# Performance work log

Hardware: AMD Instinct MI355X
Metric: run time of the kernel (lower is better)

## Reference

```python
import jax, jax.numpy as jnp
import numpy as np

N = 8192
F_IN = 690
F_OUT = 690
H = 3
ALPHA = 0.2  # LeakyReLU negative slope
NEG_INF = -9e15


def setup_inputs() -> dict:
    key = jax.random.key(0)
    k1, k2, k3, k4 = jax.random.split(key, 4)
    x = jax.random.normal(k1, (N, F_IN), dtype=jnp.float32)
    adj = jax.random.randint(k2, (N, N), 0, 2, dtype=jnp.int32)
    adj = adj.at[jnp.arange(N), jnp.arange(N)].set(1)  # self-loops, as in eye() init
    # Xavier-ish scaled params, stacked over heads
    W = jax.random.normal(k3, (H, F_IN, F_OUT), dtype=jnp.float32) * 0.05
    a = jax.random.normal(k4, (H, 2 * F_OUT, 1), dtype=jnp.float32) * 0.05
    return {"x": x, "adj": adj, "W": W, "a": a}


def reference(x, adj, W, a):
    # Wh per head: [H, N, F_OUT]
    Wh = jnp.einsum('nf,hfo->hno', x, W)
    # Additive decomposition of concat-based score: e_ij = leakyrelu(a1_i + a2_j)
    a1 = jnp.einsum('hno,ho->hn', Wh, a[:, :F_OUT, 0])  # [H, N]
    a2 = jnp.einsum('hno,ho->hn', Wh, a[:, F_OUT:, 0])  # [H, N]
    e = jax.nn.leaky_relu(a1[:, :, None] + a2[:, None, :], negative_slope=ALPHA)  # [H, N, N]
    e = jnp.where(adj[None, :, :] > 0, e, NEG_INF)
    attn = jax.nn.softmax(e, axis=-1)
    h_prime = jnp.einsum('hnm,hmo->hno', attn, Wh)  # [H, N, F_OUT]
    # GAT(concat=False): mean over heads, then ELU (dropout is identity in eval)
    y = jax.nn.elu(jnp.mean(h_prime, axis=0))  # [N, F_OUT]
    return y
```

## Files before the change

kernel.cpp:

```cpp
#include <hip/hip_runtime.h>
#include <hip/hip_bf16.h>
#include <stdint.h>

#define NN 8192
#define FD 690
#define NH 3
#define KPAD 704
#define OPAD 768
#define USTRIDE 704
#define KS 2
#define LOG2E 1.4426950408889634f

typedef __attribute__((ext_vector_type(8))) short bf16x8;
typedef __attribute__((ext_vector_type(4))) float f32x4;

typedef __attribute__((address_space(1))) const void gas_t;
typedef __attribute__((address_space(3))) void las_t;

__device__ __forceinline__ void async_ld16(const void* g, void* l) {
  __builtin_amdgcn_global_load_lds((gas_t*)g, (las_t*)l, 16, 0, 0);
}

__device__ __forceinline__ float bf2f(unsigned short u) {
  return __uint_as_float(((unsigned int)u) << 16);
}
__device__ __forceinline__ unsigned short f2bf(float f) {
  __hip_bfloat16 h = __float2bfloat16(f);
  return *reinterpret_cast<unsigned short*>(&h);
}
__device__ __forceinline__ float selbit(float e, uint32_t lo, uint32_t hi) {
  uint64_t m = ((uint64_t)hi << 32) | lo;
  float r;
  asm("v_cndmask_b32 %0, 0, %1, %2" : "=v"(r) : "v"(e), "s"(m));
  return r;
}

__global__ __launch_bounds__(256) void k_cast_x(const float* __restrict__ x,
                                                unsigned short* __restrict__ xb) {
  int idx = blockIdx.x * 256 + threadIdx.x;
  if (idx >= NN * KPAD) return;
  int n = idx / KPAD, f = idx - n * KPAD;
  float v = (f < FD) ? x[(size_t)n * FD + f] : 0.f;
  xb[idx] = f2bf(v);
}

__global__ __launch_bounds__(256) void k_cast_wt(const float* __restrict__ W,
                                                 unsigned short* __restrict__ wt) {
  int idx = blockIdx.x * 256 + threadIdx.x;
  if (idx >= NH * OPAD * KPAD) return;
  int h = idx / (OPAD * KPAD);
  int rem = idx - h * OPAD * KPAD;
  int o = rem / KPAD, f = rem - o * KPAD;
  float v = (o < FD && f < FD) ? W[((size_t)h * FD + f) * FD + o] : 0.f;
  wt[idx] = f2bf(v);
}

__global__ __launch_bounds__(256) void k_pack(const int* __restrict__ adj,
                                              uint64_t* __restrict__ bm) {
  int wid = (blockIdx.x * 256 + threadIdx.x) >> 6;
  int lane = threadIdx.x & 63;
  int i = wid >> 7, wj = wid & 127;
  int v = adj[(int64_t)i * NN + wj * 64 + lane];
  uint64_t m = __ballot(v > 0);
  if (lane == 0) bm[i * 128 + wj] = m;
}

__global__ __launch_bounds__(512) void k_gemm_wht(const unsigned short* __restrict__ wt,
                                                  const unsigned short* __restrict__ xb,
                                                  const float* __restrict__ a,
                                                  unsigned short* __restrict__ wht,
                                                  float* __restrict__ a1acc,
                                                  float* __restrict__ a2acc) {
  const int m0 = blockIdx.x * 128;
  const int n0 = blockIdx.y * 256;
  const int h  = blockIdx.z;
  const int tid = threadIdx.x;
  const int w = tid >> 6, l = tid & 63;
  const int wm = w >> 2, wn = w & 3;
  __shared__ unsigned short As[128 * 64];
  __shared__ unsigned short Bs[256 * 64];
  const unsigned short* Ag = wt + (size_t)h * OPAD * KPAD;
  f32x4 acc[4][4] = {};
  for (int kt = 0; kt < KPAD / 64; ++kt) {
    const int k0 = kt * 64;
#pragma unroll
    for (int r = 0; r < 2; ++r) {
      const unsigned short* g = Ag + (size_t)(m0 + r * 64 + w * 8 + (l >> 3)) * KPAD + k0 + (l & 7) * 8;
      async_ld16(g, &As[(r * 64 + w * 8) * 64]);
    }
#pragma unroll
    for (int r = 0; r < 4; ++r) {
      const unsigned short* g = xb + (size_t)(n0 + r * 64 + w * 8 + (l >> 3)) * KPAD + k0 + (l & 7) * 8;
      async_ld16(g, &Bs[(r * 64 + w * 8) * 64]);
    }
    __syncthreads();
#pragma unroll
    for (int ks = 0; ks < 2; ++ks) {
      bf16x8 af[4], bfr[4];
#pragma unroll
      for (int mi = 0; mi < 4; ++mi)
        af[mi] = *reinterpret_cast<const bf16x8*>(
            &As[(wm * 64 + mi * 16 + (l & 15)) * 64 + ks * 32 + (l >> 4) * 8]);
#pragma unroll
      for (int ni = 0; ni < 4; ++ni)
        bfr[ni] = *reinterpret_cast<const bf16x8*>(
            &Bs[(wn * 64 + ni * 16 + (l & 15)) * 64 + ks * 32 + (l >> 4) * 8]);
#pragma unroll
      for (int mi = 0; mi < 4; ++mi)
#pragma unroll
        for (int ni = 0; ni < 4; ++ni)
          acc[mi][ni] = __builtin_amdgcn_mfma_f32_16x16x32_bf16(af[mi], bfr[ni], acc[mi][ni], 0, 0, 0);
    }
    __syncthreads();
  }
  unsigned short* Wh = wht + (size_t)h * OPAD * NN;
#pragma unroll
  for (int mi = 0; mi < 4; ++mi)
#pragma unroll
    for (int j = 0; j < 4; ++j) {
      int o = m0 + wm * 64 + mi * 16 + (l >> 4) * 4 + j;
#pragma unroll
      for (int ni = 0; ni < 4; ++ni) {
        int n = n0 + wn * 64 + ni * 16 + (l & 15);
        float val = (o == FD) ? 1.0f : acc[mi][ni][j];
        Wh[(size_t)o * NN + n] = f2bf(val);
      }
    }
  const float* ap1 = a + h * 2 * FD;
  const float* ap2 = ap1 + FD;
  float av1[4][4], av2[4][4];
#pragma unroll
  for (int mi = 0; mi < 4; ++mi)
#pragma unroll
    for (int j = 0; j < 4; ++j) {
      int o = m0 + wm * 64 + mi * 16 + (l >> 4) * 4 + j;
      bool ok = (o < FD);
      av1[mi][j] = ok ? ap1[o] : 0.f;
      av2[mi][j] = ok ? ap2[o] : 0.f;
    }
#pragma unroll
  for (int ni = 0; ni < 4; ++ni) {
    float p1 = 0.f, p2 = 0.f;
#pragma unroll
    for (int mi = 0; mi < 4; ++mi)
#pragma unroll
      for (int j = 0; j < 4; ++j) {
        p1 += acc[mi][ni][j] * av1[mi][j];
        p2 += acc[mi][ni][j] * av2[mi][j];
      }
    int n = n0 + wn * 64 + ni * 16 + (l & 15);
    unsafeAtomicAdd(&a1acc[h * NN + n], p1);
    unsafeAtomicAdd(&a2acc[h * NN + n], p2);
  }
}

__global__ __launch_bounds__(256) void k_exp(const float* __restrict__ a1acc,
                                             const float* __restrict__ a2acc,
                                             float* __restrict__ e1s, float* __restrict__ f1s,
                                             float* __restrict__ e2s, float* __restrict__ f2s) {
  int i = blockIdx.x * 256 + threadIdx.x;
  if (i >= NH * NN) return;
  float s1 = a1acc[i] * LOG2E, s2 = a2acc[i] * LOG2E;
  e1s[i] = exp2f(s1);
  f1s[i] = exp2f(0.2f * s1);
  e2s[i] = exp2f(s2);
  f2s[i] = exp2f(0.2f * s2);
}

__global__ __launch_bounds__(512, 4) void k_pv(const unsigned short* __restrict__ wht,
                                               const float* __restrict__ e1s,
                                               const float* __restrict__ f1s,
                                               const float* __restrict__ e2s,
                                               const float* __restrict__ f2s,
                                               const uint64_t* __restrict__ bm,
                                               float* __restrict__ U) {
  const int m0 = blockIdx.x * 64;
  const int n0 = blockIdx.y * 384;
  const int h    = blockIdx.z / KS;
  const int kseg = blockIdx.z % KS;
  const int tid = threadIdx.x;
  const int w = tid >> 6, l = tid & 63;
  const int wu = __builtin_amdgcn_readfirstlane(w);
  __shared__ unsigned short As[64 * 64];
  __shared__ unsigned short Bs[384 * 64];
  const unsigned short* Bg = wht + (size_t)h * OPAD * NN;
  const uint64_t* bmw = bm + (size_t)(m0 + wu * 8) * 128;
  float E1v[8], F1v[8];
#pragma unroll
  for (int r = 0; r < 8; ++r) {
    E1v[r] = e1s[h * NN + m0 + wu * 8 + r];
    F1v[r] = f1s[h * NN + m0 + wu * 8 + r];
  }

  const int kt0 = kseg * (NN / 64 / KS);
  const int ktend = kt0 + NN / 64 / KS;

  f32x4 acc[4][3] = {};

  for (int kt = kt0; kt < ktend; ++kt) {
    const int k0 = kt * 64;
    const float e2v = e2s[h * NN + k0 + l];
    const float f2v = f2s[h * NN + k0 + l];
#pragma unroll
    for (int call = 0; call < 6; ++call) {
      int c = call * 512 + tid;
      int row = c >> 3;
      int kb  = c & 7;
      int kbs = kb ^ (row & 7);
      const unsigned short* g = Bg + (size_t)(n0 + row) * NN + k0 + kbs * 8;
      async_ld16(g, &Bs[(size_t)c * 8]);
    }
#pragma unroll
    for (int r = 0; r < 8; ++r) {
      uint64_t mrow = bmw[(size_t)r * 128 + kt];
      uint32_t mlo = __builtin_amdgcn_readfirstlane((uint32_t)mrow);
      uint32_t mhi = __builtin_amdgcn_readfirstlane((uint32_t)(mrow >> 32));
      float e = fmaxf(E1v[r] * e2v, F1v[r] * f2v);
      e = selbit(e, mlo, mhi);
      As[(wu * 8 + r) * 64 + (l ^ (r << 3))] = f2bf(e);
    }
    __syncthreads();

#pragma unroll
    for (int ks = 0; ks < 2; ++ks) {
      bf16x8 af[4], bfr[3];
#pragma unroll
      for (int mi = 0; mi < 4; ++mi) {
        int row = mi * 16 + (l & 15);
        af[mi] = *reinterpret_cast<const bf16x8*>(
            &As[row * 64 + (((ks * 4 + (l >> 4)) ^ (row & 7)) * 8)]);
      }
#pragma unroll
      for (int ni = 0; ni < 3; ++ni) {
        int row = w * 48 + ni * 16 + (l & 15);
        bfr[ni] = *reinterpret_cast<const bf16x8*>(
            &Bs[row * 64 + (((ks * 4 + (l >> 4)) ^ (row & 7)) * 8)]);
      }
#pragma unroll
      for (int mi = 0; mi < 4; ++mi)
#pragma unroll
        for (int ni = 0; ni < 3; ++ni)
          acc[mi][ni] = __builtin_amdgcn_mfma_f32_16x16x32_bf16(af[mi], bfr[ni], acc[mi][ni], 0, 0, 0);
    }
    __syncthreads();
  }

#pragma unroll
  for (int mi = 0; mi < 4; ++mi)
#pragma unroll
    for (int j = 0; j < 4; ++j) {
      int i = m0 + mi * 16 + (l >> 4) * 4 + j;
#pragma unroll
      for (int ni = 0; ni < 3; ++ni) {
        int n = n0 + w * 48 + ni * 16 + (l & 15);
        if (n <= FD) unsafeAtomicAdd(&U[((size_t)h * NN + i) * USTRIDE + n], acc[mi][ni][j]);
      }
    }
}

__global__ __launch_bounds__(256) void k_final(const float* __restrict__ U,
                                               float* __restrict__ y) {
  int idx = blockIdx.x * 256 + threadIdx.x;
  if (idx >= NN * FD) return;
  int i = idx / FD, o = idx - i * FD;
  const size_t HS = (size_t)NN * USTRIDE;
  float s = 0.f;
#pragma unroll
  for (int h = 0; h < NH; ++h) {
    size_t b = h * HS + (size_t)i * USTRIDE;
    s += U[b + o] / U[b + FD];
  }
  s *= (1.f / 3.f);
  y[idx] = s > 0.f ? s : (expf(s) - 1.f);
}

extern "C" void kernel_launch(void* const* d_in, const int* in_sizes, int n_in,
                              void* d_out, int out_size, void* d_ws, size_t ws_size,
                              hipStream_t stream) {
  const float* x   = (const float*)d_in[0];
  const int*   adj = (const int*)d_in[1];
  const float* W   = (const float*)d_in[2];
  const float* a   = (const float*)d_in[3];
  float* y = (float*)d_out;

  char* ws = (char*)d_ws;
  size_t off = 0;
  auto alloc = [&](size_t bytes) {
    void* p = ws + off;
    off = (off + bytes + 255) & ~(size_t)255;
    return p;
  };
  unsigned short* xb  = (unsigned short*)alloc((size_t)NN * KPAD * 2);
  unsigned short* wt  = (unsigned short*)alloc((size_t)NH * OPAD * KPAD * 2);
  unsigned short* wht = (unsigned short*)alloc((size_t)NH * OPAD * NN * 2);
  float* e1s = (float*)alloc((size_t)NH * NN * 4);
  float* f1s = (float*)alloc((size_t)NH * NN * 4);
  float* e2s = (float*)alloc((size_t)NH * NN * 4);
  float* f2s = (float*)alloc((size_t)NH * NN * 4);
  uint64_t* bm = (uint64_t*)alloc((size_t)NN * 128 * 8);
  float* U = (float*)alloc((size_t)NH * NN * USTRIDE * 4);
  float* a1acc = (float*)alloc((size_t)NH * NN * 4);
  float* a2acc = (float*)alloc((size_t)NH * NN * 4);
  (void)ws_size; (void)in_sizes; (void)n_in; (void)out_size;

  hipMemsetAsync(U, 0, (size_t)NH * NN * USTRIDE * 4, stream);
  hipMemsetAsync(a1acc, 0, (size_t)NH * NN * 4 * 2, stream);

  k_cast_x<<<(NN * KPAD + 255) / 256, 256, 0, stream>>>(x, xb);
  k_cast_wt<<<(NH * OPAD * KPAD + 255) / 256, 256, 0, stream>>>(W, wt);
  k_pack<<<NN * 128 / 4, 256, 0, stream>>>(adj, bm);
  k_gemm_wht<<<dim3(OPAD / 128, NN / 256, NH), 512, 0, stream>>>(wt, xb, a, wht, a1acc, a2acc);
  k_exp<<<(NH * NN + 255) / 256, 256, 0, stream>>>(a1acc, a2acc, e1s, f1s, e2s, f2s);
  k_pv<<<dim3(NN / 64, 2, NH * KS), 512, 0, stream>>>(wht, e1s, f1s, e2s, f2s, bm, U);
  k_final<<<(NN * FD + 255) / 256, 256, 0, stream>>>(U, y);
}
```

Measured before the change: 643.0 us.

## Drop split-K, double-buffer A tile, and load B fragments directly from global

Removes the K split in the attention-times-Wh kernel so each block owns a full row range and writes results with plain stores, eliminating atomics and the zero-fill memset of U. The softmax-weight tile is generated into a double-buffered LDS array one step ahead, halving barriers per iteration. B fragments are now read straight from global memory into registers rather than staged through LDS. This trades LDS traffic and atomics for exposed global load latency and half as many blocks.

```diff
diff --git a/kernel.cpp b/kernel.cpp
--- a/kernel.cpp
+++ b/kernel.cpp
@@ -8,7 +8,6 @@
 #define KPAD 704
 #define OPAD 768
 #define USTRIDE 704
-#define KS 2
 #define LOG2E 1.4426950408889634f
 
 typedef __attribute__((ext_vector_type(8))) short bf16x8;
@@ -176,13 +175,11 @@
                                                float* __restrict__ U) {
   const int m0 = blockIdx.x * 64;
   const int n0 = blockIdx.y * 384;
-  const int h    = blockIdx.z / KS;
-  const int kseg = blockIdx.z % KS;
+  const int h  = blockIdx.z;
   const int tid = threadIdx.x;
   const int w = tid >> 6, l = tid & 63;
   const int wu = __builtin_amdgcn_readfirstlane(w);
-  __shared__ unsigned short As[64 * 64];
-  __shared__ unsigned short Bs[384 * 64];
+  __shared__ unsigned short As[2][64 * 64];
   const unsigned short* Bg = wht + (size_t)h * OPAD * NN;
   const uint64_t* bmw = bm + (size_t)(m0 + wu * 8) * 128;
   float E1v[8], F1v[8];
@@ -191,25 +188,12 @@
     E1v[r] = e1s[h * NN + m0 + wu * 8 + r];
     F1v[r] = f1s[h * NN + m0 + wu * 8 + r];
   }
-
-  const int kt0 = kseg * (NN / 64 / KS);
-  const int ktend = kt0 + NN / 64 / KS;
-
-  f32x4 acc[4][3] = {};
-
-  for (int kt = kt0; kt < ktend; ++kt) {
-    const int k0 = kt * 64;
-    const float e2v = e2s[h * NN + k0 + l];
-    const float f2v = f2s[h * NN + k0 + l];
-#pragma unroll
-    for (int call = 0; call < 6; ++call) {
-      int c = call * 512 + tid;
-      int row = c >> 3;
-      int kb  = c & 7;
-      int kbs = kb ^ (row & 7);
-      const unsigned short* g = Bg + (size_t)(n0 + row) * NN + k0 + kbs * 8;
-      async_ld16(g, &Bs[(size_t)c * 8]);
-    }
+  const unsigned short* bptr[3];
+#pragma unroll
+  for (int ni = 0; ni < 3; ++ni)
+    bptr[ni] = Bg + (size_t)(n0 + w * 48 + ni * 16 + (l & 15)) * NN + (l >> 4) * 8;
+
+  auto genA = [&](int buf, int kt, float e2v, float f2v) {
 #pragma unroll
     for (int r = 0; r < 8; ++r) {
       uint64_t mrow = bmw[(size_t)r * 128 + kt];
@@ -217,24 +201,40 @@
       uint32_t mhi = __builtin_amdgcn_readfirstlane((uint32_t)(mrow >> 32));
       float e = fmaxf(E1v[r] * e2v, F1v[r] * f2v);
       e = selbit(e, mlo, mhi);
-      As[(wu * 8 + r) * 64 + (l ^ (r << 3))] = f2bf(e);
-    }
+      As[buf][(wu * 8 + r) * 64 + (l ^ (r << 3))] = f2bf(e);
+    }
+  };
+
+  f32x4 acc[4][3] = {};
+
+  float e2c = e2s[h * NN + l];
+  float f2c = f2s[h * NN + l];
+  genA(0, 0, e2c, f2c);
+  float e2n = e2s[h * NN + 64 + l];
+  float f2n = f2s[h * NN + 64 + l];
+
+  int cur = 0;
+  for (int kt = 0; kt < 128; ++kt) {
     __syncthreads();
-
+    const int k0 = kt * 64;
+    float e2nn = 0.f, f2nn = 0.f;
+    if (kt + 2 < 128) {
+      e2nn = e2s[h * NN + (kt + 2) * 64 + l];
+      f2nn = f2s[h * NN + (kt + 2) * 64 + l];
+    }
+    if (kt + 1 < 128) genA(cur ^ 1, kt + 1, e2n, f2n);
 #pragma unroll
     for (int ks = 0; ks < 2; ++ks) {
-      bf16x8 af[4], bfr[3];
+      bf16x8 bfr[3];
+#pragma unroll
+      for (int ni = 0; ni < 3; ++ni)
+        bfr[ni] = *reinterpret_cast<const bf16x8*>(bptr[ni] + k0 + ks * 32);
+      bf16x8 af[4];
 #pragma unroll
       for (int mi = 0; mi < 4; ++mi) {
         int row = mi * 16 + (l & 15);
         af[mi] = *reinterpret_cast<const bf16x8*>(
-            &As[row * 64 + (((ks * 4 + (l >> 4)) ^ (row & 7)) * 8)]);
-      }
-#pragma unroll
-      for (int ni = 0; ni < 3; ++ni) {
-        int row = w * 48 + ni * 16 + (l & 15);
-        bfr[ni] = *reinterpret_cast<const bf16x8*>(
-            &Bs[row * 64 + (((ks * 4 + (l >> 4)) ^ (row & 7)) * 8)]);
+            &As[cur][row * 64 + (((ks * 4 + (l >> 4)) ^ (row & 7)) * 8)]);
       }
 #pragma unroll
       for (int mi = 0; mi < 4; ++mi)
@@ -242,7 +242,9 @@
         for (int ni = 0; ni < 3; ++ni)
           acc[mi][ni] = __builtin_amdgcn_mfma_f32_16x16x32_bf16(af[mi], bfr[ni], acc[mi][ni], 0, 0, 0);
     }
-    __syncthreads();
+    cur ^= 1;
+    e2n = e2nn;
+    f2n = f2nn;
   }
 
 #pragma unroll
@@ -253,7 +255,7 @@
 #pragma unroll
       for (int ni = 0; ni < 3; ++ni) {
         int n = n0 + w * 48 + ni * 16 + (l & 15);
-        if (n <= FD) unsafeAtomicAdd(&U[((size_t)h * NN + i) * USTRIDE + n], acc[mi][ni][j]);
+        if (n <= FD) U[((size_t)h * NN + i) * USTRIDE + n] = acc[mi][ni][j];
       }
     }
 }
@@ -303,7 +305,6 @@
   float* a2acc = (float*)alloc((size_t)NH * NN * 4);
   (void)ws_size; (void)in_sizes; (void)n_in; (void)out_size;
 
-  hipMemsetAsync(U, 0, (size_t)NH * NN * USTRIDE * 4, stream);
   hipMemsetAsync(a1acc, 0, (size_t)NH * NN * 4 * 2, stream);
 
   k_cast_x<<<(NN * KPAD + 255) / 256, 256, 0, stream>>>(x, xb);
@@ -311,6 +312,6 @@
   k_pack<<<NN * 128 / 4, 256, 0, stream>>>(adj, bm);
   k_gemm_wht<<<dim3(OPAD / 128, NN / 256, NH), 512, 0, stream>>>(wt, xb, a, wht, a1acc, a2acc);
   k_exp<<<(NH * NN + 255) / 256, 256, 0, stream>>>(a1acc, a2acc, e1s, f1s, e2s, f2s);
-  k_pv<<<dim3(NN / 64, 2, NH * KS), 512, 0, stream>>>(wht, e1s, f1s, e2s, f2s, bm, U);
+  k_pv<<<dim3(NN / 64, 2, NH), 512, 0, stream>>>(wht, e1s, f1s, e2s, f2s, bm, U);
   k_final<<<(NN * FD + 255) / 256, 256, 0, stream>>>(U, y);
 }
```

New measurement: 824.9 us. 28.3% more time.

## Retile attention-value GEMM to 256x128 blocks with vectorized score generation

Applied to the files above, without the earlier changes.

Reshapes the k_pv tile from 64 rows x 384 columns to 256 rows x 128 columns. Waves are arranged 4x2, the K split grows from 2 to 4 segments, and the occupancy hint drops to 2 blocks. The attention-score tile is now built with vectorized loads of e2/f2 and mask words, each lane writing four bf16 values, in place of per-row scalar writes with readfirstlane masks. The aim is more MFMA work per byte of Wh loaded. In exchange, the exp/mask scores are recomputed across 6 column blocks instead of 2, and there are twice as many atomic adds into U.

```diff
diff --git a/kernel.cpp b/kernel.cpp
--- a/kernel.cpp
+++ b/kernel.cpp
@@ -8,7 +8,7 @@
 #define KPAD 704
 #define OPAD 768
 #define USTRIDE 704
-#define KS 2
+#define KS 4
 #define LOG2E 1.4426950408889634f
 
 typedef __attribute__((ext_vector_type(8))) short bf16x8;
@@ -27,12 +27,6 @@
 __device__ __forceinline__ unsigned short f2bf(float f) {
   __hip_bfloat16 h = __float2bfloat16(f);
   return *reinterpret_cast<unsigned short*>(&h);
-}
-__device__ __forceinline__ float selbit(float e, uint32_t lo, uint32_t hi) {
-  uint64_t m = ((uint64_t)hi << 32) | lo;
-  float r;
-  asm("v_cndmask_b32 %0, 0, %1, %2" : "=v"(r) : "v"(e), "s"(m));
-  return r;
 }
 
 __global__ __launch_bounds__(256) void k_cast_x(const float* __restrict__ x,
@@ -167,42 +161,48 @@
   f2s[i] = exp2f(0.2f * s2);
 }
 
-__global__ __launch_bounds__(512, 4) void k_pv(const unsigned short* __restrict__ wht,
+__global__ __launch_bounds__(512, 2) void k_pv(const unsigned short* __restrict__ wht,
                                                const float* __restrict__ e1s,
                                                const float* __restrict__ f1s,
                                                const float* __restrict__ e2s,
                                                const float* __restrict__ f2s,
                                                const uint64_t* __restrict__ bm,
                                                float* __restrict__ U) {
-  const int m0 = blockIdx.x * 64;
-  const int n0 = blockIdx.y * 384;
+  const int m0 = blockIdx.x * 256;
+  const int n0 = blockIdx.y * 128;
   const int h    = blockIdx.z / KS;
   const int kseg = blockIdx.z % KS;
   const int tid = threadIdx.x;
   const int w = tid >> 6, l = tid & 63;
-  const int wu = __builtin_amdgcn_readfirstlane(w);
-  __shared__ unsigned short As[64 * 64];
-  __shared__ unsigned short Bs[384 * 64];
+  const int wm = w >> 1, wn = w & 1;
+  __shared__ unsigned short As[256 * 64];
+  __shared__ unsigned short Bs[128 * 64];
   const unsigned short* Bg = wht + (size_t)h * OPAD * NN;
-  const uint64_t* bmw = bm + (size_t)(m0 + wu * 8) * 128;
-  float E1v[8], F1v[8];
-#pragma unroll
-  for (int r = 0; r < 8; ++r) {
-    E1v[r] = e1s[h * NN + m0 + wu * 8 + r];
-    F1v[r] = f1s[h * NN + m0 + wu * 8 + r];
-  }
-
-  const int kt0 = kseg * (NN / 64 / KS);
-  const int ktend = kt0 + NN / 64 / KS;
-
-  f32x4 acc[4][3] = {};
+
+  float E1p[8], F1p[8];
+#pragma unroll
+  for (int s = 0; s < 8; ++s) {
+    int row = m0 + w * 32 + s * 4 + (l >> 4);
+    E1p[s] = e1s[h * NN + row];
+    F1p[s] = f1s[h * NN + row];
+  }
+
+  const int kt0 = kseg * (128 / KS);
+  const int ktend = kt0 + 128 / KS;
+
+  f32x4 acc[4][4] = {};
 
   for (int kt = kt0; kt < ktend; ++kt) {
     const int k0 = kt * 64;
-    const float e2v = e2s[h * NN + k0 + l];
-    const float f2v = f2s[h * NN + k0 + l];
-#pragma unroll
-    for (int call = 0; call < 6; ++call) {
+    const f32x4 e2v = *reinterpret_cast<const f32x4*>(&e2s[h * NN + k0 + (l & 15) * 4]);
+    const f32x4 f2v = *reinterpret_cast<const f32x4*>(&f2s[h * NN + k0 + (l & 15) * 4]);
+    uint2 mr[8];
+#pragma unroll
+    for (int s = 0; s < 8; ++s)
+      mr[s] = *reinterpret_cast<const uint2*>(
+          &bm[(size_t)(m0 + w * 32 + s * 4 + (l >> 4)) * 128 + kt]);
+#pragma unroll
+    for (int call = 0; call < 2; ++call) {
       int c = call * 512 + tid;
       int row = c >> 3;
       int kb  = c & 7;
@@ -211,36 +211,51 @@
       async_ld16(g, &Bs[(size_t)c * 8]);
     }
 #pragma unroll
-    for (int r = 0; r < 8; ++r) {
-      uint64_t mrow = bmw[(size_t)r * 128 + kt];
-      uint32_t mlo = __builtin_amdgcn_readfirstlane((uint32_t)mrow);
-      uint32_t mhi = __builtin_amdgcn_readfirstlane((uint32_t)(mrow >> 32));
-      float e = fmaxf(E1v[r] * e2v, F1v[r] * f2v);
-      e = selbit(e, mlo, mhi);
-      As[(wu * 8 + r) * 64 + (l ^ (r << 3))] = f2bf(e);
+    for (int s = 0; s < 8; ++s) {
+      int row = w * 32 + s * 4 + (l >> 4);
+      uint32_t half = ((l & 15) < 8) ? mr[s].x : mr[s].y;
+      uint32_t m4 = (half >> (((l & 15) & 7) * 4)) & 0xF;
+      uint32_t lo, hi;
+      {
+        float e0 = fmaxf(E1p[s] * e2v[0], F1p[s] * f2v[0]);
+        float e1 = fmaxf(E1p[s] * e2v[1], F1p[s] * f2v[1]);
+        e0 = (m4 & 1u) ? e0 : 0.f;
+        e1 = (m4 & 2u) ? e1 : 0.f;
+        lo = (uint32_t)f2bf(e0) | ((uint32_t)f2bf(e1) << 16);
+      }
+      {
+        float e2_ = fmaxf(E1p[s] * e2v[2], F1p[s] * f2v[2]);
+        float e3 = fmaxf(E1p[s] * e2v[3], F1p[s] * f2v[3]);
+        e2_ = (m4 & 4u) ? e2_ : 0.f;
+        e3 = (m4 & 8u) ? e3 : 0.f;
+        hi = (uint32_t)f2bf(e2_) | ((uint32_t)f2bf(e3) << 16);
+      }
+      int kb = (l & 15) >> 1;
+      int phys = kb ^ (row & 7);
+      int addr = row * 64 + phys * 8 + ((l & 15) & 1) * 4;
+      uint2 val; val.x = lo; val.y = hi;
+      *reinterpret_cast<uint2*>(&As[addr]) = val;
     }
     __syncthreads();
 
 #pragma unroll
     for (int ks = 0; ks < 2; ++ks) {
-      bf16x8 af[4], bfr[3];
+      bf16x8 bfr[4];
+#pragma unroll
+      for (int ni = 0; ni < 4; ++ni) {
+        int row = wn * 64 + ni * 16 + (l & 15);
+        int phys = (ks * 4 + (l >> 4)) ^ (row & 7);
+        bfr[ni] = *reinterpret_cast<const bf16x8*>(&Bs[row * 64 + phys * 8]);
+      }
 #pragma unroll
       for (int mi = 0; mi < 4; ++mi) {
-        int row = mi * 16 + (l & 15);
-        af[mi] = *reinterpret_cast<const bf16x8*>(
-            &As[row * 64 + (((ks * 4 + (l >> 4)) ^ (row & 7)) * 8)]);
-      }
-#pragma unroll
-      for (int ni = 0; ni < 3; ++ni) {
-        int row = w * 48 + ni * 16 + (l & 15);
-        bfr[ni] = *reinterpret_cast<const bf16x8*>(
-            &Bs[row * 64 + (((ks * 4 + (l >> 4)) ^ (row & 7)) * 8)]);
-      }
-#pragma unroll
-      for (int mi = 0; mi < 4; ++mi)
-#pragma unroll
-        for (int ni = 0; ni < 3; ++ni)
-          acc[mi][ni] = __builtin_amdgcn_mfma_f32_16x16x32_bf16(af[mi], bfr[ni], acc[mi][ni], 0, 0, 0);
+        int arow = wm * 64 + mi * 16 + (l & 15);
+        int aphys = (ks * 4 + (l >> 4)) ^ (arow & 7);
+        bf16x8 af = *reinterpret_cast<const bf16x8*>(&As[arow * 64 + aphys * 8]);
+#pragma unroll
+        for (int ni = 0; ni < 4; ++ni)
+          acc[mi][ni] = __builtin_amdgcn_mfma_f32_16x16x32_bf16(af, bfr[ni], acc[mi][ni], 0, 0, 0);
+      }
     }
     __syncthreads();
   }
@@ -249,10 +264,10 @@
   for (int mi = 0; mi < 4; ++mi)
 #pragma unroll
     for (int j = 0; j < 4; ++j) {
-      int i = m0 + mi * 16 + (l >> 4) * 4 + j;
-#pragma unroll
-      for (int ni = 0; ni < 3; ++ni) {
-        int n = n0 + w * 48 + ni * 16 + (l & 15);
+      int i = m0 + wm * 64 + mi * 16 + (l >> 4) * 4 + j;
+#pragma unroll
+      for (int ni = 0; ni < 4; ++ni) {
+        int n = n0 + wn * 64 + ni * 16 + (l & 15);
         if (n <= FD) unsafeAtomicAdd(&U[((size_t)h * NN + i) * USTRIDE + n], acc[mi][ni][j]);
       }
     }
@@ -311,6 +326,6 @@
   k_pack<<<NN * 128 / 4, 256, 0, stream>>>(adj, bm);
   k_gemm_wht<<<dim3(OPAD / 128, NN / 256, NH), 512, 0, stream>>>(wt, xb, a, wht, a1acc, a2acc);
   k_exp<<<(NH * NN + 255) / 256, 256, 0, stream>>>(a1acc, a2acc, e1s, f1s, e2s, f2s);
-  k_pv<<<dim3(NN / 64, 2, NH * KS), 512, 0, stream>>>(wht, e1s, f1s, e2s, f2s, bm, U);
+  k_pv<<<dim3(NN / 256, OPAD / 128, NH * KS), 512, 0, stream>>>(wht, e1s, f1s, e2s, f2s, bm, U);
   k_final<<<(NN * FD + 255) / 256, 256, 0, stream>>>(U, y);
 }
```

Result: slower. 1.423 ms (+121.3%).
